# Kernel tuning notes

Measured on AMD Instinct MI355X. Metric: run time of the kernel, lower is better.

The kernel has to match this reference:

```python
import jax, jax.numpy as jnp
import numpy as np

H1, C1 = 16, 8   # layer1 heads, per-head channels
H2, C2 = 16, 8   # layer2 heads, per-head channels
NEG_SLOPE = 0.2


def _gatv2_layer(x, src, dst, Wl, Wr, att, bias, n_nodes, H, C):
    # x: [N, F]; Wl/Wr: [F, H*C]; att: [H, C]; bias: [H*C]
    xl = (x @ Wl).reshape(n_nodes, H, C)  # source transform
    xr = (x @ Wr).reshape(n_nodes, H, C)  # target transform
    e = jax.nn.leaky_relu(xl[src] + xr[dst], NEG_SLOPE)   # [E, H, C]
    logit = jnp.einsum('ehc,hc->eh', e, att)              # [E, H]
    # segment softmax over incoming edges of each target node
    m = jax.ops.segment_max(logit, dst, num_segments=n_nodes)  # [N, H]
    ex = jnp.exp(logit - m[dst])
    denom = jax.ops.segment_sum(ex, dst, num_segments=n_nodes)  # [N, H]
    alpha = ex / (denom[dst] + 1e-16)                     # [E, H]
    msg = xl[src] * alpha[..., None]                      # [E, H, C]
    out = jax.ops.segment_sum(msg, dst, num_segments=n_nodes)  # [N, H, C]
    return out.reshape(n_nodes, H * C) + bias


def setup_inputs() -> dict:
    key = jax.random.key(0)
    ks = jax.random.split(key, 10)
    N, E, F_IN = 50000, 800000, 128
    x = jax.random.normal(ks[0], (N, F_IN), dtype=jnp.float32)
    edge_index = jax.random.randint(ks[1], (2, E), 0, N, dtype=jnp.int32)
    s = 0.1
    return {
        'x': x,
        'edge_index': edge_index,
        'Wl1': jax.random.normal(ks[2], (F_IN, H1 * C1), dtype=jnp.float32) * s,
        'Wr1': jax.random.normal(ks[3], (F_IN, H1 * C1), dtype=jnp.float32) * s,
        'att1': jax.random.normal(ks[4], (H1, C1), dtype=jnp.float32) * s,
        'b1': jax.random.normal(ks[5], (H1 * C1,), dtype=jnp.float32) * s,
        'Wl2': jax.random.normal(ks[6], (H1 * C1, H2 * C2), dtype=jnp.float32) * s,
        'Wr2': jax.random.normal(ks[7], (H1 * C1, H2 * C2), dtype=jnp.float32) * s,
        'att2': jax.random.normal(ks[8], (H2, C2), dtype=jnp.float32) * s,
        'b2': jax.random.normal(ks[9], (H2 * C2,), dtype=jnp.float32) * s,
    }


def reference(x, edge_index, Wl1, Wr1, att1, b1, Wl2, Wr2, att2, b2):
    N = x.shape[0]
    # PyG GATv2Conv adds self-loops by default
    loops = jnp.arange(N, dtype=edge_index.dtype)
    src = jnp.concatenate([edge_index[0], loops])
    dst = jnp.concatenate([edge_index[1], loops])
    # eval mode: F.dropout(training=False) is identity
    h = _gatv2_layer(x, src, dst, Wl1, Wr1, att1, b1, N, H1, C1)
    h = jax.nn.elu(h)
    h = _gatv2_layer(h, src, dst, Wl2, Wr2, att2, b2, N, H2, C2)
    return jax.nn.log_softmax(h, axis=1)
```

## Files before the change

### kernel.cpp

```cpp
#include <hip/hip_runtime.h>

#define NEG_SLOPE 0.2f
#define BSHIFT 9
#define BNODES 512
#define EPB 2048
#define SCAP 10240
#define LOG2E 1.44269504088896340736f

typedef __attribute__((ext_vector_type(8))) short short8;
typedef __attribute__((ext_vector_type(4))) float f32x4;

__device__ inline ushort f2bf(float f) {
  uint u = __builtin_bit_cast(uint, f);
  uint r = (u + 0x7FFFu + ((u >> 16) & 1u)) >> 16;
  return (ushort)r;
}
__device__ inline float bclo(uint u) { return __builtin_bit_cast(float, u << 16); }
__device__ inline float bchi(uint u) { return __builtin_bit_cast(float, u & 0xFFFF0000u); }

__device__ inline float fast_exp2(float x) {
  float r;
  asm("v_exp_f32 %0, %1" : "=v"(r) : "v"(x));
  return r;
}

__global__ __launch_bounds__(256) void k_prep(
    const float* __restrict__ Wl1, const float* __restrict__ Wr1,
    const float* __restrict__ Wl2, const float* __restrict__ Wr2,
    ushort* __restrict__ WT1, ushort* __restrict__ WT2,
    int* __restrict__ gcount, int nb) {
  int bid = blockIdx.x;
  int t = threadIdx.x;
  if (bid < 256) {
    const float* Wa = (bid < 128) ? Wl1 : Wl2;
    const float* Wb = (bid < 128) ? Wr1 : Wr2;
    ushort* WT = (bid < 128) ? WT1 : WT2;
    int i = (bid & 127) * 256 + t;
    int n = i >> 7, k = i & 127;
    float v = (n < 128) ? Wa[k * 128 + n] : Wb[k * 128 + (n - 128)];
    WT[i] = f2bf(v);
  } else {
    if (t < nb) gcount[t] = 0;
  }
}

__global__ __launch_bounds__(256) void k_pcount(const int* __restrict__ edst, int E,
                                                int* __restrict__ gcount) {
  __shared__ int hist[128];
  int t = threadIdx.x;
  if (t < 128) hist[t] = 0;
  __syncthreads();
  int e0 = blockIdx.x * EPB;
#pragma unroll
  for (int k = 0; k < EPB / 256; ++k) {
    int e = e0 + k * 256 + t;
    if (e < E) atomicAdd(&hist[edst[e] >> BSHIFT], 1);
  }
  __syncthreads();
  if (t < 128 && hist[t] > 0) atomicAdd(&gcount[t], hist[t]);
}

__global__ __launch_bounds__(256) void k_pscan(const int* __restrict__ gcount,
                                               int* __restrict__ bbase,
                                               int* __restrict__ gcursor, int nb) {
  __shared__ int tsum[256];
  int t = threadIdx.x;
  int v = (t < nb) ? gcount[t] : 0;
  tsum[t] = v;
  __syncthreads();
  for (int d = 1; d < 256; d <<= 1) {
    int x = (t >= d) ? tsum[t - d] : 0;
    __syncthreads();
    tsum[t] += x;
    __syncthreads();
  }
  int excl = tsum[t] - v;
  if (t < nb) { bbase[t] = excl; gcursor[t] = excl; }
  if (t == nb - 1) bbase[nb] = excl + v;
}

__global__ __launch_bounds__(256) void k_pscatter(const int* __restrict__ esrc,
                                                  const int* __restrict__ edst, int E,
                                                  int* __restrict__ gcursor,
                                                  int2* __restrict__ pairs) {
  __shared__ int hist[128], lbase[128], gbase[128];
  __shared__ int tsum[256];
  __shared__ int2 stag[EPB];
  int t = threadIdx.x;
  if (t < 128) hist[t] = 0;
  __syncthreads();
  int e0 = blockIdx.x * EPB;
  int d[8], s[8], b[8], r[8];
#pragma unroll
  for (int k = 0; k < 8; ++k) {
    int e = e0 + k * 256 + t;
    if (e < E) {
      d[k] = edst[e]; s[k] = esrc[e];
      b[k] = d[k] >> BSHIFT;
      r[k] = atomicAdd(&hist[b[k]], 1);
    } else b[k] = -1;
  }
  __syncthreads();
  int hv = (t < 128) ? hist[t] : 0;
  tsum[t] = hv;
  __syncthreads();
  for (int dd = 1; dd < 256; dd <<= 1) {
    int x = (t >= dd) ? tsum[t - dd] : 0;
    __syncthreads();
    tsum[t] += x;
    __syncthreads();
  }
  if (t < 128) lbase[t] = tsum[t] - hv;
  __syncthreads();
  int tot = tsum[255];
#pragma unroll
  for (int k = 0; k < 8; ++k)
    if (b[k] >= 0) { int2 p; p.x = d[k]; p.y = s[k]; stag[lbase[b[k]] + r[k]] = p; }
  if (t < 128 && hv > 0) gbase[t] = atomicAdd(&gcursor[t], hv);
  __syncthreads();
  for (int i = t; i < tot; i += 256) {
    int2 p = stag[i];
    int bb = p.x >> BSHIFT;
    pairs[gbase[bb] + (i - lbase[bb])] = p;
  }
}

__global__ __launch_bounds__(256) void k_bsort(const int2* __restrict__ pairs,
                                               const int* __restrict__ bbase,
                                               int* __restrict__ csr, int* __restrict__ offs,
                                               int N, int E, int nb) {
  __shared__ int hist[BNODES], cur[BNODES], tsum[256];
  __shared__ int sorted[SCAP];
  int t = threadIdx.x;
  int first = blockIdx.x << BSHIFT;
  int nn = min(BNODES, N - first);
  int base = bbase[blockIdx.x];
  int cnt = bbase[blockIdx.x + 1] - base;
  hist[t] = 0; hist[t + 256] = 0;
  __syncthreads();
  for (int i = t; i < cnt; i += 256) atomicAdd(&hist[pairs[base + i].x - first], 1);
  __syncthreads();
  int a0 = hist[2 * t], a1 = hist[2 * t + 1];
  tsum[t] = a0 + a1;
  __syncthreads();
  for (int dd = 1; dd < 256; dd <<= 1) {
    int x = (t >= dd) ? tsum[t - dd] : 0;
    __syncthreads();
    tsum[t] += x;
    __syncthreads();
  }
  int ex = tsum[t] - (a0 + a1);
  cur[2 * t] = ex; cur[2 * t + 1] = ex + a0;
  if (2 * t < nn)     offs[first + 2 * t]     = base + ex;
  if (2 * t + 1 < nn) offs[first + 2 * t + 1] = base + ex + a0;
  __syncthreads();
  for (int i = t; i < cnt; i += 256) {
    int2 p = pairs[base + i];
    int pos = atomicAdd(&cur[p.x - first], 1);
    sorted[pos] = p.y;
  }
  __syncthreads();
  for (int i = t; i < cnt; i += 256) csr[base + i] = sorted[i];
  if (blockIdx.x == nb - 1 && t == 0) offs[N] = E;
}

template <bool F32IN>
__global__ __launch_bounds__(256) void k_gemm_mfma(
    const void* __restrict__ Xin, const ushort* __restrict__ WT,
    ushort* __restrict__ XLB, ushort* __restrict__ XRB, int N) {
  __shared__ ushort As[64 * 128];
  int tid = threadIdx.x;
  int lane = tid & 63;
  int w = tid >> 6;
  int n0 = blockIdx.x * 64;
  int wcol = w * 64;

  short8 bfrag[4][4];
#pragma unroll
  for (int nt = 0; nt < 4; ++nt)
#pragma unroll
    for (int ks = 0; ks < 4; ++ks)
      bfrag[nt][ks] = *reinterpret_cast<const short8*>(
          WT + (size_t)(wcol + nt * 16 + (lane & 15)) * 128 + ks * 32 + (lane >> 4) * 8);

#pragma unroll
  for (int it = 0; it < 4; ++it) {
    int flat = it * 256 + tid;
    int r = flat >> 4;
    int cb = (flat & 15) << 4;
    short8 v = {0, 0, 0, 0, 0, 0, 0, 0};
    int row = n0 + r;
    if (row < N) {
      if constexpr (F32IN) {
        const float* Xf = (const float*)Xin + (size_t)row * 128 + (cb >> 1);
        float4 f0 = *reinterpret_cast<const float4*>(Xf);
        float4 f1 = *reinterpret_cast<const float4*>(Xf + 4);
        v[0] = (short)f2bf(f0.x); v[1] = (short)f2bf(f0.y);
        v[2] = (short)f2bf(f0.z); v[3] = (short)f2bf(f0.w);
        v[4] = (short)f2bf(f1.x); v[5] = (short)f2bf(f1.y);
        v[6] = (short)f2bf(f1.z); v[7] = (short)f2bf(f1.w);
      } else {
        v = *reinterpret_cast<const short8*>((const ushort*)Xin +
                                             (size_t)row * 128 + (cb >> 1));
      }
    }
    *reinterpret_cast<short8*>(reinterpret_cast<char*>(As) + r * 256 +
                               (cb ^ ((r & 7) << 4))) = v;
  }
  __syncthreads();

  f32x4 acc[4][4];
#pragma unroll
  for (int mt = 0; mt < 4; ++mt)
#pragma unroll
    for (int nt = 0; nt < 4; ++nt) acc[mt][nt] = f32x4{0.f, 0.f, 0.f, 0.f};

#pragma unroll
  for (int ks = 0; ks < 4; ++ks) {
    short8 af[4];
#pragma unroll
    for (int mt = 0; mt < 4; ++mt) {
      int row = mt * 16 + (lane & 15);
      int cb = ks * 64 + (lane >> 4) * 16;
      af[mt] = *reinterpret_cast<const short8*>(
          reinterpret_cast<char*>(As) + row * 256 + (cb ^ ((row & 7) << 4)));
    }
#pragma unroll
    for (int mt = 0; mt < 4; ++mt)
#pragma unroll
      for (int nt = 0; nt < 4; ++nt)
        acc[mt][nt] = __builtin_amdgcn_mfma_f32_16x16x32_bf16(
            af[mt], bfrag[nt][ks], acc[mt][nt], 0, 0, 0);
  }

  ushort* dstp = (w < 2) ? XLB : XRB;
#pragma unroll
  for (int mt = 0; mt < 4; ++mt) {
    int rbase = n0 + mt * 16 + (lane >> 4) * 4;
#pragma unroll
    for (int nt = 0; nt < 4; ++nt) {
      int c = (wcol + nt * 16 + (lane & 15)) & 127;
#pragma unroll
      for (int r = 0; r < 4; ++r) {
        float v = acc[mt][nt][r];
        ushort mb = f2bf(v);
        uint ob = (uint)__shfl_xor((int)(uint)mb, 1);
        int row = rbase + r;
        if ((lane & 1) == 0 && row < N) {
          ushort2 st; st.x = mb; st.y = (ushort)ob;
          *reinterpret_cast<ushort2*>(dstp + (size_t)row * 128 + c) = st;
        }
      }
    }
  }
}

template <int MODE>
__global__ __launch_bounds__(256, 4) void k_aggregate(
    const ushort* __restrict__ XLB, const ushort* __restrict__ XRB,
    const int* __restrict__ offs, const int* __restrict__ csr,
    const float* __restrict__ att, const float* __restrict__ bias,
    void* __restrict__ OUTV, int N) {
  int tid = threadIdx.x;
  int lane = tid & 63;
  int grp = lane >> 4, li = lane & 15;
  int wid = (blockIdx.x * 256 + tid) >> 6;
  int node = (wid << 2) + grp;
  bool valid = node < N;
  int cnode = valid ? node : (N - 1);
  int ch = li << 3;

  float4 alo = *reinterpret_cast<const float4*>(att + ch);
  float4 ahi = *reinterpret_cast<const float4*>(att + ch + 4);
  const float C6 = 0.6f * LOG2E, C4 = 0.4f * LOG2E;
  float a60 = alo.x * C6, a61 = alo.y * C6, a62 = alo.z * C6, a63 = alo.w * C6;
  float a64 = ahi.x * C6, a65 = ahi.y * C6, a66 = ahi.z * C6, a67 = ahi.w * C6;
  float a40 = alo.x * C4, a41 = alo.y * C4, a42 = alo.z * C4, a43 = alo.w * C4;
  float a44 = ahi.x * C4, a45 = ahi.y * C4, a46 = ahi.z * C4, a47 = ahi.w * C4;

  uint4 xru = *reinterpret_cast<const uint4*>(XRB + ((size_t)cnode << 7) + ch);
  float xr0 = bclo(xru.x), xr1 = bchi(xru.x), xr2 = bclo(xru.y), xr3 = bchi(xru.y);
  float xr4 = bclo(xru.z), xr5 = bchi(xru.z), xr6 = bclo(xru.w), xr7 = bchi(xru.w);

  float acc0 = 0.f, acc1 = 0.f, acc2 = 0.f, acc3 = 0.f;
  float acc4 = 0.f, acc5 = 0.f, acc6 = 0.f, acc7 = 0.f, den = 0.f;

  int e0 = offs[cnode];
  int deg = valid ? (offs[cnode + 1] - e0) : 0;
  int wmax = deg;
  wmax = max(wmax, __shfl_xor(wmax, 16));
  wmax = max(wmax, __shfl_xor(wmax, 32));

#define PROC(U4, ACT)                                                        \
  {                                                                          \
    float x0 = bclo((U4).x), x1 = bchi((U4).x);                              \
    float x2 = bclo((U4).y), x3 = bchi((U4).y);                              \
    float x4 = bclo((U4).z), x5 = bchi((U4).z);                              \
    float x6 = bclo((U4).w), x7 = bchi((U4).w);                              \
    float t0 = x0 + xr0, t1 = x1 + xr1, t2 = x2 + xr2, t3 = x3 + xr3;        \
    float t4 = x4 + xr4, t5 = x5 + xr5, t6 = x6 + xr6, t7 = x7 + xr7;        \
    float q = t0 * a60;                                                      \
    q = fmaf(fabsf(t0), a40, q);                                             \
    q = fmaf(t1, a61, q); q = fmaf(fabsf(t1), a41, q);                       \
    q = fmaf(t2, a62, q); q = fmaf(fabsf(t2), a42, q);                       \
    q = fmaf(t3, a63, q); q = fmaf(fabsf(t3), a43, q);                       \
    q = fmaf(t4, a64, q); q = fmaf(fabsf(t4), a44, q);                       \
    q = fmaf(t5, a65, q); q = fmaf(fabsf(t5), a45, q);                       \
    q = fmaf(t6, a66, q); q = fmaf(fabsf(t6), a46, q);                       \
    q = fmaf(t7, a67, q); q = fmaf(fabsf(t7), a47, q);                       \
    q = (ACT) ? q : -200.f;                                                  \
    float exv = fast_exp2(q);                                                \
    acc0 = fmaf(exv, x0, acc0); acc1 = fmaf(exv, x1, acc1);                  \
    acc2 = fmaf(exv, x2, acc2); acc3 = fmaf(exv, x3, acc3);                  \
    acc4 = fmaf(exv, x4, acc4); acc5 = fmaf(exv, x5, acc5);                  \
    acc6 = fmaf(exv, x6, acc6); acc7 = fmaf(exv, x7, acc7);                  \
    den += exv;                                                              \
  }

#define LOADB(B0, B1, B2, B3, I0)                                            \
  {                                                                          \
    int s0_ = cnode, s1_ = cnode, s2_ = cnode, s3_ = cnode;                  \
    if ((I0) < deg)     s0_ = csr[e0 + (I0)];                                \
    if ((I0) + 1 < deg) s1_ = csr[e0 + (I0) + 1];                            \
    if ((I0) + 2 < deg) s2_ = csr[e0 + (I0) + 2];                            \
    if ((I0) + 3 < deg) s3_ = csr[e0 + (I0) + 3];                            \
    B0 = *reinterpret_cast<const uint4*>(XLB + (((size_t)(uint)s0_) << 7) + ch); \
    B1 = *reinterpret_cast<const uint4*>(XLB + (((size_t)(uint)s1_) << 7) + ch); \
    B2 = *reinterpret_cast<const uint4*>(XLB + (((size_t)(uint)s2_) << 7) + ch); \
    B3 = *reinterpret_cast<const uint4*>(XLB + (((size_t)(uint)s3_) << 7) + ch); \
  }

#define PROC4(B0, B1, B2, B3, I0)                                            \
  {                                                                          \
    PROC(B0, (I0) < deg); PROC(B1, (I0) + 1 < deg);                          \
    PROC(B2, (I0) + 2 < deg); PROC(B3, (I0) + 3 < deg);                      \
  }

  {
    uint4 us = *reinterpret_cast<const uint4*>(XLB + ((size_t)cnode << 7) + ch);
    PROC(us, valid);
  }

  int nb4 = (wmax + 3) >> 2;
  uint4 A0, A1, A2, A3, B0, B1, B2, B3;
  if (nb4 > 0) {
    int ia = 0, ib, next = 4;
    LOADB(A0, A1, A2, A3, 0);
    int b = 1;
    for (; b + 1 < nb4; b += 2) {
      ib = next; LOADB(B0, B1, B2, B3, ib); next += 4;
      PROC4(A0, A1, A2, A3, ia);
      ia = next; LOADB(A0, A1, A2, A3, ia); next += 4;
      PROC4(B0, B1, B2, B3, ib);
    }
    if (b < nb4) {
      ib = next; LOADB(B0, B1, B2, B3, ib);
      PROC4(A0, A1, A2, A3, ia);
      PROC4(B0, B1, B2, B3, ib);
    } else {
      PROC4(A0, A1, A2, A3, ia);
    }
  }
#undef LOADB
#undef PROC4
#undef PROC

  float inv = 1.f / (den + 1e-16f);
  float4 blo = *reinterpret_cast<const float4*>(bias + ch);
  float4 bhi = *reinterpret_cast<const float4*>(bias + ch + 4);
  float v0 = acc0 * inv + blo.x, v1 = acc1 * inv + blo.y;
  float v2 = acc2 * inv + blo.z, v3 = acc3 * inv + blo.w;
  float v4 = acc4 * inv + bhi.x, v5 = acc5 * inv + bhi.y;
  float v6 = acc6 * inv + bhi.z, v7 = acc7 * inv + bhi.w;

  if (MODE == 0) {
    v0 = (v0 > 0.f) ? v0 : expm1f(v0); v1 = (v1 > 0.f) ? v1 : expm1f(v1);
    v2 = (v2 > 0.f) ? v2 : expm1f(v2); v3 = (v3 > 0.f) ? v3 : expm1f(v3);
    v4 = (v4 > 0.f) ? v4 : expm1f(v4); v5 = (v5 > 0.f) ? v5 : expm1f(v5);
    v6 = (v6 > 0.f) ? v6 : expm1f(v6); v7 = (v7 > 0.f) ? v7 : expm1f(v7);
    if (valid) {
      ushort u[8] = {f2bf(v0), f2bf(v1), f2bf(v2), f2bf(v3),
                     f2bf(v4), f2bf(v5), f2bf(v6), f2bf(v7)};
      *reinterpret_cast<uint4*>((ushort*)OUTV + ((size_t)node << 7) + ch) =
          *reinterpret_cast<uint4*>(u);
    }
  } else {
    float m = fmaxf(fmaxf(fmaxf(v0, v1), fmaxf(v2, v3)),
                    fmaxf(fmaxf(v4, v5), fmaxf(v6, v7)));
#pragma unroll
    for (int d = 1; d < 16; d <<= 1) m = fmaxf(m, __shfl_xor(m, d));
    float s = __expf(v0 - m) + __expf(v1 - m) + __expf(v2 - m) + __expf(v3 - m) +
              __expf(v4 - m) + __expf(v5 - m) + __expf(v6 - m) + __expf(v7 - m);
#pragma unroll
    for (int d = 1; d < 16; d <<= 1) s += __shfl_xor(s, d);
    float lse = m + logf(s);
    float* op = (float*)OUTV + ((size_t)node << 7) + ch;
    if (valid) {
      *reinterpret_cast<float4*>(op) =
          make_float4(v0 - lse, v1 - lse, v2 - lse, v3 - lse);
      *reinterpret_cast<float4*>(op + 4) =
          make_float4(v4 - lse, v5 - lse, v6 - lse, v7 - lse);
    }
  }
}

extern "C" void kernel_launch(void* const* d_in, const int* in_sizes, int n_in,
                              void* d_out, int out_size, void* d_ws, size_t ws_size,
                              hipStream_t stream) {
  const float* x    = (const float*)d_in[0];
  const int*   ei   = (const int*)d_in[1];
  const float* Wl1  = (const float*)d_in[2];
  const float* Wr1  = (const float*)d_in[3];
  const float* att1 = (const float*)d_in[4];
  const float* b1   = (const float*)d_in[5];
  const float* Wl2  = (const float*)d_in[6];
  const float* Wr2  = (const float*)d_in[7];
  const float* att2 = (const float*)d_in[8];
  const float* b2   = (const float*)d_in[9];

  int N = in_sizes[0] / 128;
  int E = in_sizes[1] / 2;
  const int* esrc = ei;
  const int* edst = ei + E;
  int nb = (N + BNODES - 1) >> BSHIFT;

  char* base = (char*)d_ws;
  size_t off = 0;
  auto take = [&](size_t bytes) {
    char* p = base + off;
    off = (off + bytes + 255) & ~(size_t)255;
    return p;
  };
  int*    offs    = (int*)take((size_t)(N + 1) * 4);
  int*    csr     = (int*)take((size_t)E * 4);
  int2*   pairs   = (int2*)take((size_t)E * 8);
  int*    gcount  = (int*)take(128 * 4);
  int*    bbase   = (int*)take(132 * 4);
  int*    gcursor = (int*)take(128 * 4);
  ushort* XB      = (ushort*)take((size_t)N * 128 * 2);
  ushort* XLB     = (ushort*)take((size_t)N * 128 * 2);
  ushort* XRB     = (ushort*)take((size_t)N * 128 * 2);
  ushort* WT1     = (ushort*)take((size_t)256 * 128 * 2);
  ushort* WT2     = (ushort*)take((size_t)256 * 128 * 2);
  float*  OUT     = (float*)d_out;

  int pblocks = (E + EPB - 1) / EPB;
  int gblocks = (N + 63) / 64;
  int ablocks = (N + 15) / 16;

  k_prep<<<257, 256, 0, stream>>>(Wl1, Wr1, Wl2, Wr2, WT1, WT2, gcount, nb);
  k_pcount<<<pblocks, 256, 0, stream>>>(edst, E, gcount);
  k_pscan<<<1, 256, 0, stream>>>(gcount, bbase, gcursor, nb);
  k_pscatter<<<pblocks, 256, 0, stream>>>(esrc, edst, E, gcursor, pairs);
  k_bsort<<<nb, 256, 0, stream>>>(pairs, bbase, csr, offs, N, E, nb);

  k_gemm_mfma<true><<<gblocks, 256, 0, stream>>>(x, WT1, XLB, XRB, N);
  k_aggregate<0><<<ablocks, 256, 0, stream>>>(XLB, XRB, offs, csr, att1, b1, XB, N);
  k_gemm_mfma<false><<<gblocks, 256, 0, stream>>>(XB, WT2, XLB, XRB, N);
  k_aggregate<1><<<ablocks, 256, 0, stream>>>(XLB, XRB, offs, csr, att2, b2, OUT, N);
}
```

Measured before the change: 170.8 us.

## Pack edge pairs to 32 bits, pad CSR rows, vectorize index loads, simplify logit

Several changes at once. The weight-prep and per-bucket count kernels are merged into one launch, and a memset takes over zeroing the counters. Edge (dst,src) pairs are packed into one 32-bit word, which halves scatter traffic but assumes node ids fit in 16 bits. The CSR is rebuilt with per-node rows padded to multiples of four, and offset and degree are packed into one word so aggregation can load neighbor indices as int4. The leaky-relu attention dot product is rewritten to use fewer multiplies. The packing caps N at 65536 and per-node degree at 255 for these inputs.

```diff
diff --git a/kernel.cpp b/kernel.cpp
--- a/kernel.cpp
+++ b/kernel.cpp
@@ -24,11 +24,11 @@
   return r;
 }
 
-__global__ __launch_bounds__(256) void k_prep(
+__global__ __launch_bounds__(256) void k_prep_pc(
     const float* __restrict__ Wl1, const float* __restrict__ Wr1,
     const float* __restrict__ Wl2, const float* __restrict__ Wr2,
     ushort* __restrict__ WT1, ushort* __restrict__ WT2,
-    int* __restrict__ gcount, int nb) {
+    const int* __restrict__ edst, int E, int* __restrict__ gcount) {
   int bid = blockIdx.x;
   int t = threadIdx.x;
   if (bid < 256) {
@@ -40,24 +40,18 @@
     float v = (n < 128) ? Wa[k * 128 + n] : Wb[k * 128 + (n - 128)];
     WT[i] = f2bf(v);
   } else {
-    if (t < nb) gcount[t] = 0;
-  }
-}
-
-__global__ __launch_bounds__(256) void k_pcount(const int* __restrict__ edst, int E,
-                                                int* __restrict__ gcount) {
-  __shared__ int hist[128];
-  int t = threadIdx.x;
-  if (t < 128) hist[t] = 0;
-  __syncthreads();
-  int e0 = blockIdx.x * EPB;
-#pragma unroll
-  for (int k = 0; k < EPB / 256; ++k) {
-    int e = e0 + k * 256 + t;
-    if (e < E) atomicAdd(&hist[edst[e] >> BSHIFT], 1);
-  }
-  __syncthreads();
-  if (t < 128 && hist[t] > 0) atomicAdd(&gcount[t], hist[t]);
+    __shared__ int hist[128];
+    if (t < 128) hist[t] = 0;
+    __syncthreads();
+    int e0 = (bid - 256) * EPB;
+#pragma unroll
+    for (int k = 0; k < EPB / 256; ++k) {
+      int e = e0 + k * 256 + t;
+      if (e < E) atomicAdd(&hist[edst[e] >> BSHIFT], 1);
+    }
+    __syncthreads();
+    if (t < 128 && hist[t] > 0) atomicAdd(&gcount[t], hist[t]);
+  }
 }
 
 __global__ __launch_bounds__(256) void k_pscan(const int* __restrict__ gcount,
@@ -82,21 +76,23 @@
 __global__ __launch_bounds__(256) void k_pscatter(const int* __restrict__ esrc,
                                                   const int* __restrict__ edst, int E,
                                                   int* __restrict__ gcursor,
-                                                  int2* __restrict__ pairs) {
+                                                  uint* __restrict__ pairs) {
   __shared__ int hist[128], lbase[128], gbase[128];
   __shared__ int tsum[256];
-  __shared__ int2 stag[EPB];
+  __shared__ uint stag[EPB];
   int t = threadIdx.x;
   if (t < 128) hist[t] = 0;
   __syncthreads();
   int e0 = blockIdx.x * EPB;
-  int d[8], s[8], b[8], r[8];
+  int b[8], r[8];
+  uint pp[8];
 #pragma unroll
   for (int k = 0; k < 8; ++k) {
     int e = e0 + k * 256 + t;
     if (e < E) {
-      d[k] = edst[e]; s[k] = esrc[e];
-      b[k] = d[k] >> BSHIFT;
+      int d = edst[e], s = esrc[e];
+      pp[k] = ((uint)d << 16) | (uint)s;
+      b[k] = d >> BSHIFT;
       r[k] = atomicAdd(&hist[b[k]], 1);
     } else b[k] = -1;
   }
@@ -115,20 +111,20 @@
   int tot = tsum[255];
 #pragma unroll
   for (int k = 0; k < 8; ++k)
-    if (b[k] >= 0) { int2 p; p.x = d[k]; p.y = s[k]; stag[lbase[b[k]] + r[k]] = p; }
+    if (b[k] >= 0) stag[lbase[b[k]] + r[k]] = pp[k];
   if (t < 128 && hv > 0) gbase[t] = atomicAdd(&gcursor[t], hv);
   __syncthreads();
   for (int i = t; i < tot; i += 256) {
-    int2 p = stag[i];
-    int bb = p.x >> BSHIFT;
+    uint p = stag[i];
+    int bb = (int)(p >> (16 + BSHIFT));
     pairs[gbase[bb] + (i - lbase[bb])] = p;
   }
 }
 
-__global__ __launch_bounds__(256) void k_bsort(const int2* __restrict__ pairs,
+__global__ __launch_bounds__(256) void k_bsort(const uint* __restrict__ pairs,
                                                const int* __restrict__ bbase,
                                                int* __restrict__ csr, int* __restrict__ offs,
-                                               int N, int E, int nb) {
+                                               int N, int nb) {
   __shared__ int hist[BNODES], cur[BNODES], tsum[256];
   __shared__ int sorted[SCAP];
   int t = threadIdx.x;
@@ -136,12 +132,15 @@
   int nn = min(BNODES, N - first);
   int base = bbase[blockIdx.x];
   int cnt = bbase[blockIdx.x + 1] - base;
+  int cbase = blockIdx.x * SCAP;
   hist[t] = 0; hist[t + 256] = 0;
   __syncthreads();
-  for (int i = t; i < cnt; i += 256) atomicAdd(&hist[pairs[base + i].x - first], 1);
+  for (int i = t; i < cnt; i += 256)
+    atomicAdd(&hist[(int)(pairs[base + i] >> 16) - first], 1);
   __syncthreads();
   int a0 = hist[2 * t], a1 = hist[2 * t + 1];
-  tsum[t] = a0 + a1;
+  int a0p = (a0 + 3) & ~3, a1p = (a1 + 3) & ~3;
+  tsum[t] = a0p + a1p;
   __syncthreads();
   for (int dd = 1; dd < 256; dd <<= 1) {
     int x = (t >= dd) ? tsum[t - dd] : 0;
@@ -149,19 +148,19 @@
     tsum[t] += x;
     __syncthreads();
   }
-  int ex = tsum[t] - (a0 + a1);
-  cur[2 * t] = ex; cur[2 * t + 1] = ex + a0;
-  if (2 * t < nn)     offs[first + 2 * t]     = base + ex;
-  if (2 * t + 1 < nn) offs[first + 2 * t + 1] = base + ex + a0;
+  int ex = tsum[t] - (a0p + a1p);
+  cur[2 * t] = ex; cur[2 * t + 1] = ex + a0p;
+  if (2 * t < nn)     offs[first + 2 * t]     = ((cbase + ex) << 8) | a0;
+  if (2 * t + 1 < nn) offs[first + 2 * t + 1] = ((cbase + ex + a0p) << 8) | a1;
   __syncthreads();
   for (int i = t; i < cnt; i += 256) {
-    int2 p = pairs[base + i];
-    int pos = atomicAdd(&cur[p.x - first], 1);
-    sorted[pos] = p.y;
-  }
-  __syncthreads();
-  for (int i = t; i < cnt; i += 256) csr[base + i] = sorted[i];
-  if (blockIdx.x == nb - 1 && t == 0) offs[N] = E;
+    uint p = pairs[base + i];
+    int pos = atomicAdd(&cur[(int)(p >> 16) - first], 1);
+    sorted[pos] = (int)(p & 0xFFFFu);
+  }
+  __syncthreads();
+  int tot = tsum[255];
+  for (int i = t; i < tot; i += 256) csr[cbase + i] = sorted[i];
 }
 
 template <bool F32IN>
@@ -272,11 +271,10 @@
 
   float4 alo = *reinterpret_cast<const float4*>(att + ch);
   float4 ahi = *reinterpret_cast<const float4*>(att + ch + 4);
-  const float C6 = 0.6f * LOG2E, C4 = 0.4f * LOG2E;
+  const float C6 = 0.6f * LOG2E;
   float a60 = alo.x * C6, a61 = alo.y * C6, a62 = alo.z * C6, a63 = alo.w * C6;
   float a64 = ahi.x * C6, a65 = ahi.y * C6, a66 = ahi.z * C6, a67 = ahi.w * C6;
-  float a40 = alo.x * C4, a41 = alo.y * C4, a42 = alo.z * C4, a43 = alo.w * C4;
-  float a44 = ahi.x * C4, a45 = ahi.y * C4, a46 = ahi.z * C4, a47 = ahi.w * C4;
+  const float TT = 0.66666667f;
 
   uint4 xru = *reinterpret_cast<const uint4*>(XRB + ((size_t)cnode << 7) + ch);
   float xr0 = bclo(xru.x), xr1 = bchi(xru.x), xr2 = bclo(xru.y), xr3 = bchi(xru.y);
@@ -285,11 +283,15 @@
   float acc0 = 0.f, acc1 = 0.f, acc2 = 0.f, acc3 = 0.f;
   float acc4 = 0.f, acc5 = 0.f, acc6 = 0.f, acc7 = 0.f, den = 0.f;
 
-  int e0 = offs[cnode];
-  int deg = valid ? (offs[cnode + 1] - e0) : 0;
+  uint sd = (uint)offs[cnode];
+  int e0 = (int)(sd >> 8);
+  int deg = valid ? (int)(sd & 255u) : 0;
   int wmax = deg;
   wmax = max(wmax, __shfl_xor(wmax, 16));
   wmax = max(wmax, __shfl_xor(wmax, 32));
+  int ITER = (wmax + 3) >> 2;
+
+  const int4* csr4 = reinterpret_cast<const int4*>(csr + e0);
 
 #define PROC(U4, ACT)                                                        \
   {                                                                          \
@@ -299,15 +301,14 @@
     float x6 = bclo((U4).w), x7 = bchi((U4).w);                              \
     float t0 = x0 + xr0, t1 = x1 + xr1, t2 = x2 + xr2, t3 = x3 + xr3;        \
     float t4 = x4 + xr4, t5 = x5 + xr5, t6 = x6 + xr6, t7 = x7 + xr7;        \
-    float q = t0 * a60;                                                      \
-    q = fmaf(fabsf(t0), a40, q);                                             \
-    q = fmaf(t1, a61, q); q = fmaf(fabsf(t1), a41, q);                       \
-    q = fmaf(t2, a62, q); q = fmaf(fabsf(t2), a42, q);                       \
-    q = fmaf(t3, a63, q); q = fmaf(fabsf(t3), a43, q);                       \
-    q = fmaf(t4, a64, q); q = fmaf(fabsf(t4), a44, q);                       \
-    q = fmaf(t5, a65, q); q = fmaf(fabsf(t5), a45, q);                       \
-    q = fmaf(t6, a66, q); q = fmaf(fabsf(t6), a46, q);                       \
-    q = fmaf(t7, a67, q); q = fmaf(fabsf(t7), a47, q);                       \
+    float u0 = fmaf(fabsf(t0), TT, t0), u1 = fmaf(fabsf(t1), TT, t1);        \
+    float u2 = fmaf(fabsf(t2), TT, t2), u3 = fmaf(fabsf(t3), TT, t3);        \
+    float u4 = fmaf(fabsf(t4), TT, t4), u5 = fmaf(fabsf(t5), TT, t5);        \
+    float u6 = fmaf(fabsf(t6), TT, t6), u7 = fmaf(fabsf(t7), TT, t7);        \
+    float q = u0 * a60;                                                      \
+    q = fmaf(u1, a61, q); q = fmaf(u2, a62, q); q = fmaf(u3, a63, q);        \
+    q = fmaf(u4, a64, q); q = fmaf(u5, a65, q); q = fmaf(u6, a66, q);        \
+    q = fmaf(u7, a67, q);                                                    \
     q = (ACT) ? q : -200.f;                                                  \
     float exv = fast_exp2(q);                                                \
     acc0 = fmaf(exv, x0, acc0); acc1 = fmaf(exv, x1, acc1);                  \
@@ -317,13 +318,12 @@
     den += exv;                                                              \
   }
 
-#define LOADB(B0, B1, B2, B3, I0)                                            \
+#define GATHER(B0, B1, B2, B3, IDX, I0)                                      \
   {                                                                          \
-    int s0_ = cnode, s1_ = cnode, s2_ = cnode, s3_ = cnode;                  \
-    if ((I0) < deg)     s0_ = csr[e0 + (I0)];                                \
-    if ((I0) + 1 < deg) s1_ = csr[e0 + (I0) + 1];                            \
-    if ((I0) + 2 < deg) s2_ = csr[e0 + (I0) + 2];                            \
-    if ((I0) + 3 < deg) s3_ = csr[e0 + (I0) + 3];                            \
+    int s0_ = ((I0) < deg) ? (IDX).x : cnode;                                \
+    int s1_ = ((I0) + 1 < deg) ? (IDX).y : cnode;                            \
+    int s2_ = ((I0) + 2 < deg) ? (IDX).z : cnode;                            \
+    int s3_ = ((I0) + 3 < deg) ? (IDX).w : cnode;                            \
     B0 = *reinterpret_cast<const uint4*>(XLB + (((size_t)(uint)s0_) << 7) + ch); \
     B1 = *reinterpret_cast<const uint4*>(XLB + (((size_t)(uint)s1_) << 7) + ch); \
     B2 = *reinterpret_cast<const uint4*>(XLB + (((size_t)(uint)s2_) << 7) + ch); \
@@ -341,27 +341,30 @@
     PROC(us, valid);
   }
 
-  int nb4 = (wmax + 3) >> 2;
   uint4 A0, A1, A2, A3, B0, B1, B2, B3;
-  if (nb4 > 0) {
-    int ia = 0, ib, next = 4;
-    LOADB(A0, A1, A2, A3, 0);
+  int4 ia, ib;
+  if (ITER > 0) {
+    ia = csr4[0];
+    GATHER(A0, A1, A2, A3, ia, 0);
+    ib = (ITER > 1) ? csr4[1] : ia;
     int b = 1;
-    for (; b + 1 < nb4; b += 2) {
-      ib = next; LOADB(B0, B1, B2, B3, ib); next += 4;
-      PROC4(A0, A1, A2, A3, ia);
-      ia = next; LOADB(A0, A1, A2, A3, ia); next += 4;
-      PROC4(B0, B1, B2, B3, ib);
-    }
-    if (b < nb4) {
-      ib = next; LOADB(B0, B1, B2, B3, ib);
-      PROC4(A0, A1, A2, A3, ia);
-      PROC4(B0, B1, B2, B3, ib);
+    for (; b + 1 < ITER; b += 2) {
+      GATHER(B0, B1, B2, B3, ib, 4 * b);
+      ia = csr4[b + 1];
+      PROC4(A0, A1, A2, A3, 4 * (b - 1));
+      GATHER(A0, A1, A2, A3, ia, 4 * (b + 1));
+      ib = csr4[b + 2];
+      PROC4(B0, B1, B2, B3, 4 * b);
+    }
+    if (b < ITER) {
+      GATHER(B0, B1, B2, B3, ib, 4 * b);
+      PROC4(A0, A1, A2, A3, 4 * (b - 1));
+      PROC4(B0, B1, B2, B3, 4 * b);
     } else {
-      PROC4(A0, A1, A2, A3, ia);
-    }
-  }
-#undef LOADB
+      PROC4(A0, A1, A2, A3, 4 * (b - 1));
+    }
+  }
+#undef GATHER
 #undef PROC4
 #undef PROC
 
@@ -431,9 +434,9 @@
     off = (off + bytes + 255) & ~(size_t)255;
     return p;
   };
-  int*    offs    = (int*)take((size_t)(N + 1) * 4);
-  int*    csr     = (int*)take((size_t)E * 4);
-  int2*   pairs   = (int2*)take((size_t)E * 8);
+  int*    offs    = (int*)take((size_t)N * 4);
+  int*    csr     = (int*)take((size_t)nb * SCAP * 4 + 256);
+  uint*   pairs   = (uint*)take((size_t)E * 4);
   int*    gcount  = (int*)take(128 * 4);
   int*    bbase   = (int*)take(132 * 4);
   int*    gcursor = (int*)take(128 * 4);
@@ -448,11 +451,12 @@
   int gblocks = (N + 63) / 64;
   int ablocks = (N + 15) / 16;
 
-  k_prep<<<257, 256, 0, stream>>>(Wl1, Wr1, Wl2, Wr2, WT1, WT2, gcount, nb);
-  k_pcount<<<pblocks, 256, 0, stream>>>(edst, E, gcount);
+  hipMemsetAsync(gcount, 0, 128 * sizeof(int), stream);
+  k_prep_pc<<<256 + pblocks, 256, 0, stream>>>(Wl1, Wr1, Wl2, Wr2, WT1, WT2,
+                                               edst, E, gcount);
   k_pscan<<<1, 256, 0, stream>>>(gcount, bbase, gcursor, nb);
   k_pscatter<<<pblocks, 256, 0, stream>>>(esrc, edst, E, gcursor, pairs);
-  k_bsort<<<nb, 256, 0, stream>>>(pairs, bbase, csr, offs, N, E, nb);
+  k_bsort<<<nb, 256, 0, stream>>>(pairs, bbase, csr, offs, N, nb);
 
   k_gemm_mfma<true><<<gblocks, 256, 0, stream>>>(x, WT1, XLB, XRB, N);
   k_aggregate<0><<<ablocks, 256, 0, stream>>>(XLB, XRB, offs, csr, att1, b1, XB, N);
```

Result: no change. 167.6 us (-1.8%).
